# Optimization experiments

Measured on AMD Instinct MI355X. Metric: run time of the kernel, lower is better.

Reference implementation:

```python
import jax, jax.numpy as jnp
import numpy as np

BN_EPS = 1e-5
L2_EPS = 1e-8


def l2norm(x, axis=-1):
    # matches torch: x / (sqrt(sum(x^2)) + eps)
    n = jnp.sqrt(jnp.sum(x * x, axis=axis, keepdims=True)) + L2_EPS
    return x / n


def setup_inputs() -> dict:
    key = jax.random.key(0)
    ks = jax.random.split(key, 8)
    B, N, D, E = 512, 193, 512, 2048
    g = 4                      # uniform pid-group size (<= max_rows=8)
    k_tok = (N - 1) // 2       # = 96, matches DynamicLinearProjection k
    H = E // 2                 # MLP hidden = 1024
    base_features = jax.random.normal(ks[0], (B, N, D), jnp.float32)
    atten = jax.random.uniform(ks[1], (B, N, N), jnp.float32)
    pid = jnp.arange(B) // g   # contiguous groups of size g
    # dynamic projection params for group size g
    W_dyn = jax.random.normal(ks[2], (g, D), jnp.float32)          # weights[f'weight_{g}'] ~ randn
    b_dyn = jnp.zeros((g,), jnp.float32)
    W_lin = jax.random.normal(ks[3], (E, k_tok * g), jnp.float32) * 0.02  # linears[f'linear_{g}']
    b_lin = jnp.zeros((E,), jnp.float32)
    # MLP(input=512, hidden=1024, output=2048, 2 layers)
    W1 = jax.random.normal(ks[4], (H, D), jnp.float32) * 0.02
    b1 = jnp.zeros((H,), jnp.float32)
    gamma1 = jnp.ones((H,), jnp.float32)
    beta1 = jnp.zeros((H,), jnp.float32)
    W2 = jax.random.normal(ks[5], (E, H), jnp.float32) * 0.02
    b2 = jnp.zeros((E,), jnp.float32)
    return {"base_features": base_features, "atten": atten, "pid": pid,
            "W_dyn": W_dyn, "b_dyn": b_dyn, "W_lin": W_lin, "b_lin": b_lin,
            "W1": W1, "b1": b1, "gamma1": gamma1, "beta1": beta1,
            "W2": W2, "b2": b2}


def reference(base_features, atten, pid, W_dyn, b_dyn, W_lin, b_lin,
              W1, b1, gamma1, beta1, W2, b2):
    B, N, D = base_features.shape
    k_tok = (N - 1) // 2                      # 96
    g = W_dyn.shape[0]                        # uniform group size (pid = arange//g)
    G = B // g
    E = W_lin.shape[0]
    # --- top-k token selection (atten[:, :, 0] = -1, then topk over atten[:, 0, :]) ---
    scores = atten[:, 0, :].at[:, 0].set(-1.0)            # (B, N)
    _, idx = jax.lax.top_k(scores, k_tok)                 # (B, k_tok), descending
    feats = jnp.take_along_axis(base_features, idx[:, :, None], axis=1)  # (B, k_tok, D)
    # --- per-pid-group dynamic projection (uniform groups -> one batched GEMM) ---
    # torch: cat group members -> (g*k_tok, D); F.linear(x, W_dyn, b_dyn).T -> (g, g*k_tok); linear_g -> (g, E)
    Xg = feats.reshape(G, g * k_tok, D)
    y = jnp.einsum('gnd,rd->grn', Xg, W_dyn) + b_dyn[None, :, None]     # (G, g, g*k_tok)
    new_feats = jnp.einsum('gri,oi->gro', y, W_lin) + b_lin             # (G, g, E)
    # scatter: output[member_idx] = row; contiguous groups => plain reshape
    new_feats = l2norm(new_feats.reshape(B, E))
    # --- MLP branch on l2-normalized selected features ---
    x = l2norm(feats).reshape(B * k_tok, D)
    h = x @ W1.T + b1
    mu = jnp.mean(h, axis=0)
    var = jnp.var(h, axis=0)                  # biased, as torch BN training-mode
    h = (h - mu) * jax.lax.rsqrt(var + BN_EPS) * gamma1 + beta1
    h = jax.nn.relu(h)
    out = (h @ W2.T + b2).reshape(B, k_tok, E)
    pooled = jnp.max(out, axis=1)             # maxk_pool1d_var with k=1 => max over tokens
    return (pooled + new_feats).astype(jnp.float32)
```

## Files before the change

### kernel.cpp

```cpp
#include <hip/hip_runtime.h>
#include <math.h>

#define B_   512
#define N_   193
#define D_   512
#define E_   2048
#define KTOK 96
#define H_   1024
#define M1   (B_ * KTOK)
#define KGD  (KTOK * 4)

typedef _Float16 half8 __attribute__((ext_vector_type(8)));
typedef _Float16 half4v __attribute__((ext_vector_type(4)));
typedef float floatx4 __attribute__((ext_vector_type(4)));

__device__ __forceinline__ void gll16(const _Float16* g, _Float16* l) {
    __builtin_amdgcn_global_load_lds(
        (const __attribute__((address_space(1))) unsigned int*)(const void*)g,
        (__attribute__((address_space(3))) unsigned int*)(void*)l, 16, 0, 0);
}

__global__ void zero_stats_kernel(double* stats) {
    int i = blockIdx.x * 256 + threadIdx.x;
    if (i < 2 * H_) stats[i] = 0.0;
}

__global__ void topk_kernel(const float* __restrict__ atten, int* __restrict__ idx) {
    __shared__ float s[N_];
    int b = blockIdx.x;
    const float* row = atten + (size_t)b * N_ * N_;
    for (int i = threadIdx.x; i < N_; i += blockDim.x)
        s[i] = (i == 0) ? -1.0f : row[i];
    __syncthreads();
    for (int i = threadIdx.x; i < N_; i += blockDim.x) {
        float v = s[i];
        int rank = 0;
        for (int j = 0; j < N_; ++j) {
            float u = s[j];
            rank += (u > v) || (u == v && j < i);
        }
        if (rank < KTOK) idx[b * KTOK + rank] = i;
    }
}

__global__ __launch_bounds__(256) void gather_kernel(
        const float* __restrict__ base, const int* __restrict__ idx,
        const float* __restrict__ W_dyn, const float* __restrict__ b_dyn,
        _Float16* __restrict__ Xh, float* __restrict__ Y) {
    int ln = threadIdx.x & 63, wv = threadIdx.x >> 6;
    int rowid = blockIdx.x * 4 + wv;
    int b = rowid / KTOK, t = rowid - b * KTOK;
    int tok = idx[rowid];
    const float4* src = (const float4*)(base + ((size_t)b * N_ + tok) * D_);
    float4 v0 = src[ln * 2], v1 = src[ln * 2 + 1];

    float vals[5];
    vals[0] = v0.x * v0.x + v0.y * v0.y + v0.z * v0.z + v0.w * v0.w
            + v1.x * v1.x + v1.y * v1.y + v1.z * v1.z + v1.w * v1.w;
#pragma unroll
    for (int r = 0; r < 4; ++r) {
        const float4* wr = (const float4*)(W_dyn + r * D_);
        float4 w0 = wr[ln * 2], w1 = wr[ln * 2 + 1];
        vals[1 + r] = v0.x * w0.x + v0.y * w0.y + v0.z * w0.z + v0.w * w0.w
                    + v1.x * w1.x + v1.y * w1.y + v1.z * w1.z + v1.w * w1.w;
    }
#pragma unroll
    for (int c = 0; c < 5; ++c)
#pragma unroll
        for (int o = 32; o > 0; o >>= 1) vals[c] += __shfl_xor(vals[c], o, 64);

    float inv = 1.0f / (sqrtf(vals[0]) + 1e-8f);
    half8 o8;
    o8[0] = (_Float16)(v0.x * inv); o8[1] = (_Float16)(v0.y * inv);
    o8[2] = (_Float16)(v0.z * inv); o8[3] = (_Float16)(v0.w * inv);
    o8[4] = (_Float16)(v1.x * inv); o8[5] = (_Float16)(v1.y * inv);
    o8[6] = (_Float16)(v1.z * inv); o8[7] = (_Float16)(v1.w * inv);
    *(half8*)&Xh[(size_t)rowid * D_ + ln * 8] = o8;
    if (ln == 0) {
        int g = b >> 2;
        int n = (b & 3) * KTOK + t;
#pragma unroll
        for (int r = 0; r < 4; ++r)
            Y[(size_t)(g * 4 + r) * KGD + n] = vals[1 + r] + b_dyn[r];
    }
}

__global__ __launch_bounds__(256) void newfeat_kernel(
        const float* __restrict__ Y, const float* __restrict__ W_lin,
        const float* __restrict__ b_lin, float* __restrict__ NF) {
    __shared__ float sy[4][KGD];
    __shared__ float red[4][4];
    __shared__ float tot[4];
    int b0 = blockIdx.x * 4;
    int tid = threadIdx.x;
    for (int l = tid; l < 4 * KGD; l += 256)
        sy[l / KGD][l % KGD] = Y[(size_t)b0 * KGD + l];
    __syncthreads();

    float out[4][8];
    float ssq[4] = {0.f, 0.f, 0.f, 0.f};
#pragma unroll
    for (int q = 0; q < 8; ++q) {
        int o = tid + 256 * q;
        float a0 = 0.f, a1 = 0.f, a2 = 0.f, a3 = 0.f;
        const float4* wr = (const float4*)(W_lin + (size_t)o * KGD);
        for (int i4 = 0; i4 < KGD / 4; ++i4) {
            float4 w  = wr[i4];
            float4 s0 = *(const float4*)&sy[0][i4 * 4];
            float4 s1 = *(const float4*)&sy[1][i4 * 4];
            float4 s2 = *(const float4*)&sy[2][i4 * 4];
            float4 s3 = *(const float4*)&sy[3][i4 * 4];
            a0 += w.x * s0.x + w.y * s0.y + w.z * s0.z + w.w * s0.w;
            a1 += w.x * s1.x + w.y * s1.y + w.z * s1.z + w.w * s1.w;
            a2 += w.x * s2.x + w.y * s2.y + w.z * s2.z + w.w * s2.w;
            a3 += w.x * s3.x + w.y * s3.y + w.z * s3.z + w.w * s3.w;
        }
        float bl = b_lin[o];
        out[0][q] = a0 + bl; out[1][q] = a1 + bl;
        out[2][q] = a2 + bl; out[3][q] = a3 + bl;
#pragma unroll
        for (int r = 0; r < 4; ++r) ssq[r] += out[r][q] * out[r][q];
    }

    int lane = tid & 63, wid = tid >> 6;
#pragma unroll
    for (int c = 0; c < 4; ++c) {
        float v = ssq[c];
        for (int o = 32; o > 0; o >>= 1) v += __shfl_down(v, o, 64);
        if (lane == 0) red[c][wid] = v;
    }
    __syncthreads();
    if (tid < 4) tot[tid] = red[tid][0] + red[tid][1] + red[tid][2] + red[tid][3];
    __syncthreads();
#pragma unroll
    for (int r = 0; r < 4; ++r) {
        float norm = sqrtf(tot[r]) + 1e-8f;
#pragma unroll
        for (int q = 0; q < 8; ++q) {
            int o = tid + 256 * q;
            NF[(size_t)(b0 + r) * E_ + o] = out[r][q] / norm;
        }
    }
}

__global__ __launch_bounds__(256) void convw_kernel(
        const float* __restrict__ W1, const float* __restrict__ W2,
        _Float16* __restrict__ W1h, _Float16* __restrict__ W2h) {
    int i = blockIdx.x * 256 + threadIdx.x;
    if (i < 131072) {
        float4 v = *(const float4*)&W1[(size_t)i * 4];
        half4v o = {(_Float16)v.x, (_Float16)v.y, (_Float16)v.z, (_Float16)v.w};
        *(half4v*)&W1h[(size_t)i * 4] = o;
    } else {
        int j = i - 131072;
        float4 v = *(const float4*)&W2[(size_t)j * 4];
        half4v o = {(_Float16)v.x, (_Float16)v.y, (_Float16)v.z, (_Float16)v.w};
        *(half4v*)&W2h[(size_t)j * 4] = o;
    }
}

__global__ __launch_bounds__(512, 2) void gemm1s(
        const _Float16* __restrict__ A, const _Float16* __restrict__ Bm,
        const float* __restrict__ bias, _Float16* __restrict__ Cf16,
        double* __restrict__ stats) {
    constexpr int KA = 512, NS = 16, NBX = 4;
    __shared__ _Float16 Sl[4][14336];
    int tid = threadIdx.x;
    int ln = tid & 63, w = tid >> 6;
    int wr = w >> 2, wc = w & 3;
    int rid = blockIdx.x;
    int q = rid >> 3;
    int bx = q & (NBX - 1);
    int by = ((q / NBX) << 3) | (rid & 7);
    int n0 = bx * 256, m0 = by * 192;

    bool isA = (w < 4);
    const _Float16* sg[4];
    int ld[4];
    if (isA) {
#pragma unroll
        for (int i = 0; i < 3; ++i) {
            int j = w * 3 + i;
            int u = j * 64 + ln;
            int kg = u / 192, row = u - kg * 192;
            sg[i] = A + (size_t)(m0 + row) * KA + kg * 8;
            ld[i] = j * 512;
        }
        sg[3] = sg[0]; ld[3] = ld[0];
    } else {
#pragma unroll
        for (int i = 0; i < 4; ++i) {
            int j = (w - 4) * 4 + i;
            int u = j * 64 + ln;
            int kg = u >> 8, col = u & 255;
            sg[i] = Bm + (size_t)(n0 + col) * KA + kg * 8;
            ld[i] = 6144 + j * 512;
        }
    }

#define CSTAGE(s) { int ko = (s) * 32; _Float16* dst = &Sl[(s) & 3][0];        \
    if (isA) { gll16(sg[0] + ko, dst + ld[0]); gll16(sg[1] + ko, dst + ld[1]); \
               gll16(sg[2] + ko, dst + ld[2]); }                               \
    else     { gll16(sg[0] + ko, dst + ld[0]); gll16(sg[1] + ko, dst + ld[1]); \
               gll16(sg[2] + ko, dst + ld[2]); gll16(sg[3] + ko, dst + ld[3]); } }
#define WAITV(na, nb) { if (isA) asm volatile("s_waitcnt vmcnt(" #na ")" ::: "memory"); \
                        else     asm volatile("s_waitcnt vmcnt(" #nb ")" ::: "memory"); }

    int aofs[6], bofs[4];
#pragma unroll
    for (int f = 0; f < 6; ++f)
        aofs[f] = ((ln >> 4) * 192 + wr * 96 + f * 16 + (ln & 15)) * 8;
#pragma unroll
    for (int n = 0; n < 4; ++n)
        bofs[n] = 6144 + ((ln >> 4) * 256 + wc * 64 + n * 16 + (ln & 15)) * 8;

    floatx4 zero = {0.f, 0.f, 0.f, 0.f};
    floatx4 acc[6][4];
#pragma unroll
    for (int i = 0; i < 6; ++i)
#pragma unroll
        for (int j = 0; j < 4; ++j) acc[i][j] = zero;

    CSTAGE(0); CSTAGE(1); CSTAGE(2);
    WAITV(6, 8);
    __builtin_amdgcn_s_barrier();

    for (int s = 0; s < NS; ++s) {
        const _Float16* SL = &Sl[s & 3][0];
        half8 bv[4], av[6];
#pragma unroll
        for (int n = 0; n < 4; ++n) bv[n] = *(const half8*)&SL[bofs[n]];
#pragma unroll
        for (int f = 0; f < 6; ++f) av[f] = *(const half8*)&SL[aofs[f]];
        if (s + 3 < NS) CSTAGE(s + 3);
        __builtin_amdgcn_sched_barrier(0);
        asm volatile("s_waitcnt lgkmcnt(0)" ::: "memory");
        __builtin_amdgcn_sched_barrier(0);
        __builtin_amdgcn_s_setprio(1);
#pragma unroll
        for (int f = 0; f < 6; ++f)
#pragma unroll
            for (int n = 0; n < 4; ++n)
                acc[f][n] = __builtin_amdgcn_mfma_f32_16x16x32_f16(av[f], bv[n], acc[f][n], 0, 0, 0);
        __builtin_amdgcn_s_setprio(0);
        __builtin_amdgcn_sched_barrier(0);
        if (s + 1 < NS) {
            if (s + 3 < NS)      { WAITV(6, 8); }
            else if (s + 2 < NS) { WAITV(3, 4); }
            else                 { WAITV(0, 0); }
        }
        __builtin_amdgcn_s_barrier();
    }
#undef CSTAGE
#undef WAITV

    float cs[4] = {0.f, 0.f, 0.f, 0.f}, cq[4] = {0.f, 0.f, 0.f, 0.f};
#pragma unroll
    for (int f = 0; f < 6; ++f) {
        int row = m0 + wr * 96 + f * 16 + (ln >> 4) * 4;
#pragma unroll
        for (int n = 0; n < 4; ++n) {
            int col = n0 + wc * 64 + n * 16 + (ln & 15);
            float bb = bias[col];
#pragma unroll
            for (int r = 0; r < 4; ++r) {
                float v = acc[f][n][r] + bb;
                Cf16[(size_t)(row + r) * H_ + col] = (_Float16)v;
                cs[n] += v; cq[n] += v * v;
            }
        }
    }
#pragma unroll
    for (int n = 0; n < 4; ++n) {
        cs[n] += __shfl_xor(cs[n], 16); cs[n] += __shfl_xor(cs[n], 32);
        cq[n] += __shfl_xor(cq[n], 16); cq[n] += __shfl_xor(cq[n], 32);
    }
    float* sp = (float*)&Sl[0][0];
    __syncthreads();
    if (ln < 16) {
#pragma unroll
        for (int n = 0; n < 4; ++n) {
            int c = wc * 64 + n * 16 + ln;
            sp[(wr * 256 + c) * 2 + 0] = cs[n];
            sp[(wr * 256 + c) * 2 + 1] = cq[n];
        }
    }
    __syncthreads();
    if (tid < 256) {
        float s0 = sp[tid * 2]     + sp[(256 + tid) * 2];
        float q0 = sp[tid * 2 + 1] + sp[(256 + tid) * 2 + 1];
        atomicAdd(&stats[n0 + tid], (double)s0);
        atomicAdd(&stats[H_ + n0 + tid], (double)q0);
    }
}

__global__ void finalize_kernel(const double* __restrict__ stats,
                                const float* __restrict__ gamma,
                                const float* __restrict__ beta,
                                _Float16* __restrict__ scsh16) {
    int c = blockIdx.x * 256 + threadIdx.x;
    if (c >= H_) return;
    double mean = stats[c] / (double)M1;
    double var  = stats[H_ + c] / (double)M1 - mean * mean;
    float sc = gamma[c] * (float)(1.0 / sqrt(var + 1e-5));
    float sh = beta[c] - (float)mean * sc;
    scsh16[c] = (_Float16)sc;
    scsh16[H_ + c] = (_Float16)sh;
}

__device__ __forceinline__ half8 bnrelu8(half8 h, const _Float16* scp, const _Float16* shp) {
    half8 s = *(const half8*)scp, t = *(const half8*)shp, o;
#pragma unroll
    for (int e = 0; e < 8; ++e) {
        _Float16 v = h[e] * s[e] + t[e];
        o[e] = (v > (_Float16)0.f) ? v : (_Float16)0.f;
    }
    return o;
}

__global__ __launch_bounds__(512, 2) void gemm2f(
        const _Float16* __restrict__ Hb, const _Float16* __restrict__ Bm,
        const _Float16* __restrict__ scsh16, const float* __restrict__ bias,
        const float* __restrict__ NF, float* __restrict__ out) {
    constexpr int KA = 1024, NS = 32, NBX = 8;
    __shared__ _Float16 Sl[4][14336];
    __shared__ _Float16 scL[H_], shL[H_];
    int tid = threadIdx.x;
    int ln = tid & 63, w = tid >> 6;
    int wr = w >> 2, wc = w & 3;
    int rid = blockIdx.x;
    int qq = rid >> 3;
    int bx = qq & (NBX - 1);
    int by = ((qq / NBX) << 3) | (rid & 7);
    int n0 = bx * 256, m0 = by * 192;
    bool isA = (w < 4);

    for (int i = tid; i < H_; i += 512) { scL[i] = scsh16[i]; shL[i] = scsh16[H_ + i]; }

    const _Float16 *sgA0 = Hb, *sgA1 = Hb, *sgA2 = Hb;
    int ldA0 = 0, ldA1 = 0, ldA2 = 0, kgA0 = 0, kgA1 = 0, kgA2 = 0;
    const _Float16* sgB[4] = {Bm, Bm, Bm, Bm};
    int ldB[4] = {6144, 6144, 6144, 6144};
    if (isA) {
        { int j = w * 3 + 0; int u = j * 64 + ln; kgA0 = u / 192; int row = u - kgA0 * 192;
          sgA0 = Hb + (size_t)(m0 + row) * KA + kgA0 * 8; ldA0 = j * 512; }
        { int j = w * 3 + 1; int u = j * 64 + ln; kgA1 = u / 192; int row = u - kgA1 * 192;
          sgA1 = Hb + (size_t)(m0 + row) * KA + kgA1 * 8; ldA1 = j * 512; }
        { int j = w * 3 + 2; int u = j * 64 + ln; kgA2 = u / 192; int row = u - kgA2 * 192;
          sgA2 = Hb + (size_t)(m0 + row) * KA + kgA2 * 8; ldA2 = j * 512; }
    } else {
#pragma unroll
        for (int i = 0; i < 4; ++i) {
            int j = (w - 4) * 4 + i;
            int u = j * 64 + ln;
            int kg = u >> 8, col = u & 255;
            sgB[i] = Bm + (size_t)(n0 + col) * KA + kg * 8;
            ldB[i] = 6144 + j * 512;
        }
    }

#define A_ISSUE(t, Ra, Rb, Rc) { Ra = *(const half8*)(sgA0 + (size_t)(t) * 32); \
    Rb = *(const half8*)(sgA1 + (size_t)(t) * 32);                              \
    Rc = *(const half8*)(sgA2 + (size_t)(t) * 32); }
#define A_XFRM(t, Ra, Rb, Rc) { _Float16* dst = &Sl[(t) & 3][0]; int c0 = (t) * 32; \
    *(half8*)(dst + ldA0 + ln * 8) = bnrelu8(Ra, &scL[c0 + kgA0 * 8], &shL[c0 + kgA0 * 8]); \
    *(half8*)(dst + ldA1 + ln * 8) = bnrelu8(Rb, &scL[c0 + kgA1 * 8], &shL[c0 + kgA1 * 8]); \
    *(half8*)(dst + ldA2 + ln * 8) = bnrelu8(Rc, &scL[c0 + kgA2 * 8], &shL[c0 + kgA2 * 8]); }
#define B_STAGE(t) { int ko = (t) * 32; _Float16* dst = &Sl[(t) & 3][0]; \
    gll16(sgB[0] + ko, dst + ldB[0]); gll16(sgB[1] + ko, dst + ldB[1]); \
    gll16(sgB[2] + ko, dst + ldB[2]); gll16(sgB[3] + ko, dst + ldB[3]); }

    int aofs[6], bofs[4];
#pragma unroll
    for (int f = 0; f < 6; ++f)
        aofs[f] = ((ln >> 4) * 192 + wr * 96 + f * 16 + (ln & 15)) * 8;
#pragma unroll
    for (int n = 0; n < 4; ++n)
        bofs[n] = 6144 + ((ln >> 4) * 256 + wc * 64 + n * 16 + (ln & 15)) * 8;

    floatx4 zero = {0.f, 0.f, 0.f, 0.f};
    floatx4 acc[6][4];
#pragma unroll
    for (int i = 0; i < 6; ++i)
#pragma unroll
        for (int j = 0; j < 4; ++j) acc[i][j] = zero;

    half8 e0a, e0b, e0c, e1a, e1b, e1c;

    if (isA) { A_ISSUE(0, e0a, e0b, e0c); A_ISSUE(1, e1a, e1b, e1c); }
    else     { B_STAGE(0); B_STAGE(1); B_STAGE(2); }
    asm volatile("s_waitcnt lgkmcnt(0)" ::: "memory");
    __builtin_amdgcn_s_barrier();
    if (isA) {
        A_XFRM(0, e0a, e0b, e0c);
        A_ISSUE(2, e0a, e0b, e0c);
        A_XFRM(1, e1a, e1b, e1c);
    } else {
        asm volatile("s_waitcnt vmcnt(8)" ::: "memory");
    }
    asm volatile("s_waitcnt lgkmcnt(0)" ::: "memory");
    __builtin_amdgcn_s_barrier();

#define SLOT(s, Ia, Ib, Ic, Xa, Xb, Xc) {                                       \
    const _Float16* SL = &Sl[(s) & 3][0];                                       \
    half8 bv[4], av[6];                                                         \
    _Pragma("unroll") for (int n = 0; n < 4; ++n) bv[n] = *(const half8*)&SL[bofs[n]]; \
    _Pragma("unroll") for (int f = 0; f < 6; ++f) av[f] = *(const half8*)&SL[aofs[f]]; \
    if ((s) + 3 < NS) { if (isA) { A_ISSUE((s) + 3, Ia, Ib, Ic); } else { B_STAGE((s) + 3); } } \
    __builtin_amdgcn_sched_barrier(0);                                          \
    asm volatile("s_waitcnt lgkmcnt(0)" ::: "memory");                          \
    __builtin_amdgcn_sched_barrier(0);                                          \
    __builtin_amdgcn_s_setprio(1);                                              \
    _Pragma("unroll") for (int f = 0; f < 6; ++f)                               \
        _Pragma("unroll") for (int n = 0; n < 4; ++n)                           \
            acc[f][n] = __builtin_amdgcn_mfma_f32_16x16x32_f16(av[f], bv[n], acc[f][n], 0, 0, 0); \
    __builtin_amdgcn_s_setprio(0);                                              \
    if (isA) {                                                                  \
        if ((s) + 2 < NS) { A_XFRM((s) + 2, Xa, Xb, Xc); }                      \
        asm volatile("s_waitcnt lgkmcnt(0)" ::: "memory");                      \
    } else {                                                                    \
        if ((s) + 3 < NS)      { asm volatile("s_waitcnt vmcnt(8)" ::: "memory"); } \
        else if ((s) + 2 < NS) { asm volatile("s_waitcnt vmcnt(4)" ::: "memory"); } \
        else if ((s) + 1 < NS) { asm volatile("s_waitcnt vmcnt(0)" ::: "memory"); } \
    }                                                                           \
    __builtin_amdgcn_s_barrier();                                               \
}

    for (int s = 0; s < NS; s += 2) {
        SLOT(s,     e1a, e1b, e1c, e0a, e0b, e0c);
        SLOT(s + 1, e0a, e0b, e0c, e1a, e1b, e1c);
    }
#undef SLOT
#undef A_ISSUE
#undef A_XFRM
#undef B_STAGE

    int batch = by * 2 + wr;
#pragma unroll
    for (int n = 0; n < 4; ++n) {
        float m = -3.4e38f;
#pragma unroll
        for (int f = 0; f < 6; ++f)
#pragma unroll
            for (int r = 0; r < 4; ++r) m = fmaxf(m, acc[f][n][r]);
        m = fmaxf(m, __shfl_xor(m, 16));
        m = fmaxf(m, __shfl_xor(m, 32));
        if (ln < 16) {
            int col = n0 + wc * 64 + n * 16 + ln;
            out[(size_t)batch * E_ + col] = m + bias[col] + NF[(size_t)batch * E_ + col];
        }
    }
}

extern "C" void kernel_launch(void* const* d_in, const int* in_sizes, int n_in,
                              void* d_out, int out_size, void* d_ws, size_t ws_size,
                              hipStream_t stream) {
    (void)in_sizes; (void)n_in; (void)out_size; (void)ws_size;
    const float* base  = (const float*)d_in[0];
    const float* atten = (const float*)d_in[1];
    const float* W_dyn = (const float*)d_in[3];
    const float* b_dyn = (const float*)d_in[4];
    const float* W_lin = (const float*)d_in[5];
    const float* b_lin = (const float*)d_in[6];
    const float* W1    = (const float*)d_in[7];
    const float* b1    = (const float*)d_in[8];
    const float* gamma = (const float*)d_in[9];
    const float* beta  = (const float*)d_in[10];
    const float* W2    = (const float*)d_in[11];
    const float* b2    = (const float*)d_in[12];
    float* out = (float*)d_out;

    char* wsp = (char*)d_ws;
    int*      idx    = (int*)(wsp);
    float*    Y      = (float*)(wsp + 196608);
    float*    NF     = (float*)(wsp + 983040);
    double*   stats  = (double*)(wsp + 5177344);
    _Float16* scsh16 = (_Float16*)(wsp + 5193728);
    _Float16* W1h    = (_Float16*)(wsp + 5201920);
    _Float16* W2h    = (_Float16*)(wsp + 6250496);
    _Float16* Xh     = (_Float16*)(wsp + 10444800);
    _Float16* Hbh    = (_Float16*)(wsp + 60776448);

    zero_stats_kernel<<<8, 256, 0, stream>>>(stats);
    topk_kernel<<<B_, 256, 0, stream>>>(atten, idx);
    convw_kernel<<<2560, 256, 0, stream>>>(W1, W2, W1h, W2h);
    gather_kernel<<<M1 / 4, 256, 0, stream>>>(base, idx, W_dyn, b_dyn, Xh, Y);
    newfeat_kernel<<<B_ / 4, 256, 0, stream>>>(Y, W_lin, b_lin, NF);
    gemm1s<<<1024, 512, 0, stream>>>(Xh, W1h, b1, Hbh, stats);
    finalize_kernel<<<4, 256, 0, stream>>>(stats, gamma, beta, scsh16);
    gemm2f<<<2048, 512, 0, stream>>>(Hbh, W2h, scsh16, b2, NF, out);
}
```

Before: 529.1 us.

## Restructure gemm2f into 64-wide K tiles with all-wave cooperative loads and phased MFMA

```diff
diff --git a/kernel.cpp b/kernel.cpp
--- a/kernel.cpp
+++ b/kernel.cpp
@@ -322,8 +322,8 @@
         const _Float16* __restrict__ Hb, const _Float16* __restrict__ Bm,
         const _Float16* __restrict__ scsh16, const float* __restrict__ bias,
         const float* __restrict__ NF, float* __restrict__ out) {
-    constexpr int KA = 1024, NS = 32, NBX = 8;
-    __shared__ _Float16 Sl[4][14336];
+    constexpr int KA = 1024, NT = 16, NBX = 8;
+    __shared__ _Float16 Sl[2][28672];
     __shared__ _Float16 scL[H_], shL[H_];
     int tid = threadIdx.x;
     int ln = tid & 63, w = tid >> 6;
@@ -333,50 +333,50 @@
     int bx = qq & (NBX - 1);
     int by = ((qq / NBX) << 3) | (rid & 7);
     int n0 = bx * 256, m0 = by * 192;
-    bool isA = (w < 4);
 
     for (int i = tid; i < H_; i += 512) { scL[i] = scsh16[i]; shL[i] = scsh16[H_ + i]; }
 
-    const _Float16 *sgA0 = Hb, *sgA1 = Hb, *sgA2 = Hb;
-    int ldA0 = 0, ldA1 = 0, ldA2 = 0, kgA0 = 0, kgA1 = 0, kgA2 = 0;
-    const _Float16* sgB[4] = {Bm, Bm, Bm, Bm};
-    int ldB[4] = {6144, 6144, 6144, 6144};
-    if (isA) {
-        { int j = w * 3 + 0; int u = j * 64 + ln; kgA0 = u / 192; int row = u - kgA0 * 192;
-          sgA0 = Hb + (size_t)(m0 + row) * KA + kgA0 * 8; ldA0 = j * 512; }
-        { int j = w * 3 + 1; int u = j * 64 + ln; kgA1 = u / 192; int row = u - kgA1 * 192;
-          sgA1 = Hb + (size_t)(m0 + row) * KA + kgA1 * 8; ldA1 = j * 512; }
-        { int j = w * 3 + 2; int u = j * 64 + ln; kgA2 = u / 192; int row = u - kgA2 * 192;
-          sgA2 = Hb + (size_t)(m0 + row) * KA + kgA2 * 8; ldA2 = j * 512; }
-    } else {
-#pragma unroll
-        for (int i = 0; i < 4; ++i) {
-            int j = (w - 4) * 4 + i;
-            int u = j * 64 + ln;
-            int kg = u >> 8, col = u & 255;
-            sgB[i] = Bm + (size_t)(n0 + col) * KA + kg * 8;
-            ldB[i] = 6144 + j * 512;
-        }
-    }
-
-#define A_ISSUE(t, Ra, Rb, Rc) { Ra = *(const half8*)(sgA0 + (size_t)(t) * 32); \
-    Rb = *(const half8*)(sgA1 + (size_t)(t) * 32);                              \
-    Rc = *(const half8*)(sgA2 + (size_t)(t) * 32); }
-#define A_XFRM(t, Ra, Rb, Rc) { _Float16* dst = &Sl[(t) & 3][0]; int c0 = (t) * 32; \
-    *(half8*)(dst + ldA0 + ln * 8) = bnrelu8(Ra, &scL[c0 + kgA0 * 8], &shL[c0 + kgA0 * 8]); \
-    *(half8*)(dst + ldA1 + ln * 8) = bnrelu8(Rb, &scL[c0 + kgA1 * 8], &shL[c0 + kgA1 * 8]); \
-    *(half8*)(dst + ldA2 + ln * 8) = bnrelu8(Rc, &scL[c0 + kgA2 * 8], &shL[c0 + kgA2 * 8]); }
-#define B_STAGE(t) { int ko = (t) * 32; _Float16* dst = &Sl[(t) & 3][0]; \
-    gll16(sgB[0] + ko, dst + ldB[0]); gll16(sgB[1] + ko, dst + ldB[1]); \
+    const _Float16* sgA[3];
+    int ldA[3];
+#pragma unroll
+    for (int i = 0; i < 3; ++i) {
+        int row = i * 64 + ln;
+        sgA[i] = Hb + (size_t)(m0 + row) * KA + w * 8;
+        ldA[i] = (w * 192 + row) * 8;
+    }
+    const _Float16* sgB[4];
+    int ldB[4];
+#pragma unroll
+    for (int q2 = 0; q2 < 4; ++q2) {
+        int c = (q2 < 2) ? (2 * w + q2) : (16 + 2 * w + (q2 - 2));
+        int kg = c >> 2, col = (c & 3) * 64 + ln;
+        sgB[q2] = Bm + (size_t)(n0 + col) * KA + kg * 8;
+        ldB[q2] = 12288 + (kg * 256 + col) * 8;
+    }
+
+#define A_ISSUE(t, Ra, Rb, Rc) { Ra = *(const half8*)(sgA[0] + (size_t)(t) * 64); \
+    Rb = *(const half8*)(sgA[1] + (size_t)(t) * 64);                              \
+    Rc = *(const half8*)(sgA[2] + (size_t)(t) * 64); }
+#define A_XFRM(t, Ra, Rb, Rc) { _Float16* dst = &Sl[(t) & 1][0]; int c0 = (t) * 64 + w * 8; \
+    *(half8*)(dst + ldA[0]) = bnrelu8(Ra, &scL[c0], &shL[c0]); \
+    *(half8*)(dst + ldA[1]) = bnrelu8(Rb, &scL[c0], &shL[c0]); \
+    *(half8*)(dst + ldA[2]) = bnrelu8(Rc, &scL[c0], &shL[c0]); }
+#define B_STG0(t) { _Float16* dst = &Sl[(t) & 1][0]; int ko = (t) * 64; \
+    gll16(sgB[0] + ko, dst + ldB[0]); gll16(sgB[1] + ko, dst + ldB[1]); }
+#define B_STG1(t) { _Float16* dst = &Sl[(t) & 1][0]; int ko = (t) * 64; \
     gll16(sgB[2] + ko, dst + ldB[2]); gll16(sgB[3] + ko, dst + ldB[3]); }
 
-    int aofs[6], bofs[4];
+    int aofs[6][2], bofs[4][2];
 #pragma unroll
     for (int f = 0; f < 6; ++f)
-        aofs[f] = ((ln >> 4) * 192 + wr * 96 + f * 16 + (ln & 15)) * 8;
+#pragma unroll
+        for (int kh = 0; kh < 2; ++kh)
+            aofs[f][kh] = ((kh * 4 + (ln >> 4)) * 192 + wr * 96 + f * 16 + (ln & 15)) * 8;
 #pragma unroll
     for (int n = 0; n < 4; ++n)
-        bofs[n] = 6144 + ((ln >> 4) * 256 + wc * 64 + n * 16 + (ln & 15)) * 8;
+#pragma unroll
+        for (int kh = 0; kh < 2; ++kh)
+            bofs[n][kh] = 12288 + ((kh * 4 + (ln >> 4)) * 256 + wc * 64 + n * 16 + (ln & 15)) * 8;
 
     floatx4 zero = {0.f, 0.f, 0.f, 0.f};
     floatx4 acc[6][4];
@@ -385,55 +385,78 @@
 #pragma unroll
         for (int j = 0; j < 4; ++j) acc[i][j] = zero;
 
-    half8 e0a, e0b, e0c, e1a, e1b, e1c;
-
-    if (isA) { A_ISSUE(0, e0a, e0b, e0c); A_ISSUE(1, e1a, e1b, e1c); }
-    else     { B_STAGE(0); B_STAGE(1); B_STAGE(2); }
-    asm volatile("s_waitcnt lgkmcnt(0)" ::: "memory");
-    __builtin_amdgcn_s_barrier();
-    if (isA) {
-        A_XFRM(0, e0a, e0b, e0c);
-        A_ISSUE(2, e0a, e0b, e0c);
-        A_XFRM(1, e1a, e1b, e1c);
-    } else {
-        asm volatile("s_waitcnt vmcnt(8)" ::: "memory");
-    }
-    asm volatile("s_waitcnt lgkmcnt(0)" ::: "memory");
-    __builtin_amdgcn_s_barrier();
-
-#define SLOT(s, Ia, Ib, Ic, Xa, Xb, Xc) {                                       \
-    const _Float16* SL = &Sl[(s) & 3][0];                                       \
-    half8 bv[4], av[6];                                                         \
-    _Pragma("unroll") for (int n = 0; n < 4; ++n) bv[n] = *(const half8*)&SL[bofs[n]]; \
-    _Pragma("unroll") for (int f = 0; f < 6; ++f) av[f] = *(const half8*)&SL[aofs[f]]; \
-    if ((s) + 3 < NS) { if (isA) { A_ISSUE((s) + 3, Ia, Ib, Ic); } else { B_STAGE((s) + 3); } } \
-    __builtin_amdgcn_sched_barrier(0);                                          \
-    asm volatile("s_waitcnt lgkmcnt(0)" ::: "memory");                          \
-    __builtin_amdgcn_sched_barrier(0);                                          \
-    __builtin_amdgcn_s_setprio(1);                                              \
-    _Pragma("unroll") for (int f = 0; f < 6; ++f)                               \
-        _Pragma("unroll") for (int n = 0; n < 4; ++n)                           \
-            acc[f][n] = __builtin_amdgcn_mfma_f32_16x16x32_f16(av[f], bv[n], acc[f][n], 0, 0, 0); \
-    __builtin_amdgcn_s_setprio(0);                                              \
-    if (isA) {                                                                  \
-        if ((s) + 2 < NS) { A_XFRM((s) + 2, Xa, Xb, Xc); }                      \
-        asm volatile("s_waitcnt lgkmcnt(0)" ::: "memory");                      \
-    } else {                                                                    \
-        if ((s) + 3 < NS)      { asm volatile("s_waitcnt vmcnt(8)" ::: "memory"); } \
-        else if ((s) + 2 < NS) { asm volatile("s_waitcnt vmcnt(4)" ::: "memory"); } \
-        else if ((s) + 1 < NS) { asm volatile("s_waitcnt vmcnt(0)" ::: "memory"); } \
-    }                                                                           \
-    __builtin_amdgcn_s_barrier();                                               \
-}
-
-    for (int s = 0; s < NS; s += 2) {
-        SLOT(s,     e1a, e1b, e1c, e0a, e0b, e0c);
-        SLOT(s + 1, e0a, e0b, e0c, e1a, e1b, e1c);
-    }
-#undef SLOT
+    half8 e0a, e0b, e0c, o0a, o0b, o0c;
+
+#define FENCE __builtin_amdgcn_sched_barrier(0)
+#define BAR   __builtin_amdgcn_s_barrier()
+#define LGKM0 asm volatile("s_waitcnt lgkmcnt(0)" ::: "memory")
+#define PH_READA(mh, kh) { av[0] = *(const half8*)&SL[aofs[(mh) * 3 + 0][kh]]; \
+    av[1] = *(const half8*)&SL[aofs[(mh) * 3 + 1][kh]]; \
+    av[2] = *(const half8*)&SL[aofs[(mh) * 3 + 2][kh]]; }
+#define PH_READB(kh) { bv[0] = *(const half8*)&SL[bofs[0][kh]]; bv[1] = *(const half8*)&SL[bofs[1][kh]]; \
+    bv[2] = *(const half8*)&SL[bofs[2][kh]]; bv[3] = *(const half8*)&SL[bofs[3][kh]]; }
+#define PH_MFMA(mh) { _Pragma("unroll") for (int f3 = 0; f3 < 3; ++f3) \
+    _Pragma("unroll") for (int n = 0; n < 4; ++n) \
+        acc[(mh) * 3 + f3][n] = __builtin_amdgcn_mfma_f32_16x16x32_f16(av[f3], bv[n], acc[(mh) * 3 + f3][n], 0, 0, 0); }
+
+    B_STG0(0); B_STG1(0);
+    A_ISSUE(0, e0a, e0b, e0c);
+    A_ISSUE(1, o0a, o0b, o0c);
+    A_XFRM(0, e0a, e0b, e0c);
+    LGKM0;
+    BAR;
+
+#define TILE(T, Ia, Ib, Ic, Xa, Xb, Xc) { \
+    const _Float16* SL = &Sl[(T) & 1][0]; \
+    half8 av[3], bv[4]; \
+     \
+    PH_READA(0, 0); PH_READB(0); \
+    if ((T) + 1 < NT) B_STG0((T) + 1); \
+    if ((T) + 2 < NT) A_ISSUE((T) + 2, Ia, Ib, Ic); \
+    FENCE; BAR; LGKM0; FENCE; \
+    __builtin_amdgcn_s_setprio(1); PH_MFMA(0); __builtin_amdgcn_s_setprio(0); FENCE; \
+    BAR; \
+     \
+    PH_READA(1, 0); \
+    if ((T) + 1 < NT) B_STG1((T) + 1); \
+    FENCE; BAR; LGKM0; FENCE; \
+    __builtin_amdgcn_s_setprio(1); PH_MFMA(1); __builtin_amdgcn_s_setprio(0); FENCE; \
+    if ((T) + 2 < NT)      { asm volatile("s_waitcnt vmcnt(7)" ::: "memory"); } \
+    else if ((T) + 1 < NT) { asm volatile("s_waitcnt vmcnt(4)" ::: "memory"); } \
+    else                   { asm volatile("s_waitcnt vmcnt(0)" ::: "memory"); } \
+    BAR; \
+     \
+    PH_READA(0, 1); PH_READB(1); \
+    FENCE; BAR; LGKM0; FENCE; \
+    __builtin_amdgcn_s_setprio(1); PH_MFMA(0); __builtin_amdgcn_s_setprio(0); FENCE; \
+    BAR; \
+     \
+    PH_READA(1, 1); \
+    FENCE; BAR; LGKM0; FENCE; \
+    __builtin_amdgcn_s_setprio(1); PH_MFMA(1); __builtin_amdgcn_s_setprio(0); FENCE; \
+    if ((T) + 1 < NT) { \
+        A_XFRM((T) + 1, Xa, Xb, Xc); \
+        if ((T) + 2 < NT) { asm volatile("s_waitcnt vmcnt(5)" ::: "memory"); } \
+        else              { asm volatile("s_waitcnt vmcnt(2)" ::: "memory"); } \
+    } \
+    LGKM0; BAR; \
+}
+
+    for (int s = 0; s < NT; s += 2) {
+        TILE(s,     e0a, e0b, e0c, o0a, o0b, o0c);
+        TILE(s + 1, o0a, o0b, o0c, e0a, e0b, e0c);
+    }
+#undef TILE
+#undef PH_READA
+#undef PH_READB
+#undef PH_MFMA
+#undef FENCE
+#undef BAR
+#undef LGKM0
 #undef A_ISSUE
 #undef A_XFRM
-#undef B_STAGE
+#undef B_STG0
+#undef B_STG1
 
     int batch = by * 2 + wr;
 #pragma unroll
```

Measured after the change: 638.7 us. +20.7%, slower.
